# Kernel optimization log

Measured on AMD Instinct MI355X. Metric: run time of the kernel, lower is better.

The kernel has to match this reference:

```python
import jax, jax.numpy as jnp
import numpy as np

EPS = 1e-5

def _conv3x3(x, w):
    # x: [n,c,h,w], w: [o,c,3,3], stride 1, padding 1 (SAME)
    return jax.lax.conv_general_dilated(x, w, (1, 1), 'SAME',
                                        dimension_numbers=('NCHW', 'OIHW', 'NCHW'))

def _bn(x, g, b, m, v):
    # inference-mode BatchNorm2d with running stats
    s = g / jnp.sqrt(v + EPS)
    return x * s[:, None, None] + (b - m * s)[:, None, None]

def _lrelu(x):
    return jnp.where(x > 0, x, 0.2 * x)

def _conv1x1(x, w, b):
    # w: [o,c] (1x1 conv kernel collapsed)
    return jnp.einsum('nchw,oc->nohw', x, w) + b[:, None, None]

def _conv_relu(x, w, g, b, m, v):
    return _lrelu(_bn(_conv3x3(x, w), g, b, m, v))

def _pam(f, Wq, bq, Wk, bk, Wv, bv, alpha):
    n, c, h, w = f.shape
    hw = h * w
    q = _conv1x1(f, Wq, bq).reshape(n, -1, hw)   # [n,cr,hw]
    k = _conv1x1(f, Wk, bk).reshape(n, -1, hw)   # [n,cr,hw]
    # attention[i,j] over spatial tokens, softmax along j
    attn = jax.nn.softmax(jnp.einsum('nci,ncj->nij', q, k), axis=-1)  # [n,hw,hw]
    v = _conv1x1(f, Wv, bv).reshape(n, c, hw)    # [n,c,hw]
    # torch: bmm(v, attn^T) -> out[:, :, i] = sum_j v[:, :, j] * attn[i, j]
    out = jnp.einsum('ncj,nij->nci', v, attn).reshape(n, c, h, w)
    return alpha * out + f

def _cam(f, W1, b1, W2, b2):
    s = jnp.mean(f, axis=(2, 3), keepdims=True)  # AdaptiveAvgPool2d(1)
    s = _lrelu(_conv1x1(s, W1, b1))
    s = jax.nn.sigmoid(_conv1x1(s, W2, b2))
    return f * s

def _upx2(x):
    n, c, h, w = x.shape
    return jax.image.resize(x, (n, c, 2 * h, 2 * w), 'bilinear')

def setup_inputs() -> dict:
    key = jax.random.key(0)
    ks = jax.random.split(key, 16)
    N, C, H, W_ = 4, 512, 64, 64
    CR, NC = C // 8, 64
    f32 = jnp.float32
    def nrm(k, shape, s=0.05):
        return jax.random.normal(k, shape, f32) * s
    return {
        'x': jax.random.normal(ks[0], (N, C, H, W_), f32),
        'W_pam_in': nrm(ks[1], (C, C, 3, 3)),
        'pam_gamma': jnp.ones((C,), f32), 'pam_beta': jnp.zeros((C,), f32),
        'pam_mean': nrm(ks[2], (C,)), 'pam_var': jax.random.uniform(ks[3], (C,), f32) + 0.5,
        'Wq': nrm(ks[4], (CR, C)), 'bq': jnp.zeros((CR,), f32),
        'Wk': nrm(ks[5], (CR, C)), 'bk': jnp.zeros((CR,), f32),
        'Wv': nrm(ks[6], (C, C)), 'bv': jnp.zeros((C,), f32),
        'alpha': nrm(ks[7], (1,), 1.0),
        'W_pam_out': nrm(ks[8], (NC, C)), 'b_pam_out': jnp.zeros((NC,), f32),
        'W_cam_in': nrm(ks[9], (C, C, 3, 3)),
        'cam_gamma': jnp.ones((C,), f32), 'cam_beta': jnp.zeros((C,), f32),
        'cam_mean': nrm(ks[10], (C,)), 'cam_var': jax.random.uniform(ks[11], (C,), f32) + 0.5,
        'Wc1': nrm(ks[12], (CR, C)), 'bc1': jnp.zeros((CR,), f32),
        'Wc2': nrm(ks[13], (C, CR)), 'bc2': jnp.zeros((C,), f32),
        'W_cam_out': nrm(ks[14], (NC, C)), 'b_cam_out': jnp.zeros((NC,), f32),
    }

def reference(x, W_pam_in, pam_gamma, pam_beta, pam_mean, pam_var,
              Wq, bq, Wk, bk, Wv, bv, alpha, W_pam_out, b_pam_out,
              W_cam_in, cam_gamma, cam_beta, cam_mean, cam_var,
              Wc1, bc1, Wc2, bc2, W_cam_out, b_cam_out):
    pam_feat = _conv_relu(x, W_pam_in, pam_gamma, pam_beta, pam_mean, pam_var)
    pam_feat = _pam(pam_feat, Wq, bq, Wk, bk, Wv, bv, alpha)
    pam_feat = _upx2(_conv1x1(pam_feat, W_pam_out, b_pam_out))
    cam_feat = _conv_relu(x, W_cam_in, cam_gamma, cam_beta, cam_mean, cam_var)
    cam_feat = _cam(cam_feat, Wc1, bc1, Wc2, bc2)
    cam_feat = _upx2(_conv1x1(cam_feat, W_cam_out, b_cam_out))
    return pam_feat + cam_feat
```

## Files before the change

### kernel.cpp

```cpp
#include <hip/hip_runtime.h>
#include <hip/hip_bf16.h>
#include <math.h>

#define N_  4
#define C_  512
#define H_  64
#define W_  64
#define HW_ 4096
#define CR_ 64
#define NC_ 64
#define EPSV 1e-5f

typedef __attribute__((ext_vector_type(8))) __bf16 bf16x8;
typedef __attribute__((ext_vector_type(4))) float f32x4;
typedef __hip_bfloat16 bf16s;

__device__ __forceinline__ unsigned short bfb(float f) {
    union { bf16s h; unsigned short u; } cv;
    cv.h = __float2bfloat16(f);
    return cv.u;
}

__device__ __forceinline__ int swz8(int row, int ch) {
    return row * 64 + ((ch ^ (row & 7)) << 3);
}

__global__ __launch_bounds__(256) void k_xpose(
    const float* __restrict__ x, bf16s* __restrict__ xbT)
{
    __shared__ float xs[64][65];
    const int tid = threadIdx.x;
    const int n = blockIdx.z, c0 = blockIdx.y * 64, p0 = blockIdx.x * 64;
    for (int e = tid; e < 4096; e += 256) {
        int ci = e >> 6, pi = e & 63;
        xs[ci][pi] = x[((size_t)(n*C_ + c0 + ci))*HW_ + p0 + pi];
    }
    __syncthreads();
    for (int e = tid; e < 4096; e += 256) {
        int pi = e >> 6, ci = e & 63;
        xbT[((size_t)n*HW_ + p0 + pi)*C_ + c0 + ci] = __float2bfloat16(xs[ci][pi]);
    }
}

__global__ __launch_bounds__(256) void k_wprep(
    const float* __restrict__ w, bf16s* __restrict__ wb)
{
    int e = blockIdx.x * 256 + threadIdx.x;
    int c = e & 511; int r = e >> 9;
    int tap = r % 9; int o = r / 9;
    wb[e] = __float2bfloat16(w[((size_t)o*C_ + c)*9 + tap]);
}

__global__ __launch_bounds__(256) void k_wcast(
    const float* __restrict__ in, bf16s* __restrict__ out, int nElem)
{
    int e = blockIdx.x * 256 + threadIdx.x;
    if (e < nElem) out[e] = __float2bfloat16(in[e]);
}

__global__ __launch_bounds__(256, 2) void k_conv3x3_mfma(
    const bf16s* __restrict__ xbT, const bf16s* __restrict__ wb,
    const float* __restrict__ gamma, const float* __restrict__ beta,
    const float* __restrict__ mean, const float* __restrict__ var,
    float* __restrict__ out, bf16s* __restrict__ featT,
    float* __restrict__ csum, int mode)
{
    __shared__ bf16s aL[3][128][36];
    __shared__ bf16s bL[132][36];
    const int tid = threadIdx.x;
    const int n  = blockIdx.z;
    const int o0 = blockIdx.y * 128;
    const int pt = blockIdx.x;
    const int y0 = pt * 2;
    const int lane = tid & 63;
    const int wid  = tid >> 6;
    const int wr = wid >> 1, wc = wid & 1;
    const int lr = lane & 15, cb = lane >> 4;

    const int ao  = tid >> 2;
    const int ac  = (tid & 3) * 8;
    const int t0  = tid >> 2;
    const int t1  = t0 + 64;
    const int t2  = t0 + 128;
    const int ry1 = t1 >= 66 ? 1 : 0;
    const int xi1 = t1 - (ry1 ? 66 : 0);

    f32x4 acc[4][4];
#pragma unroll
    for (int i = 0; i < 4; ++i)
#pragma unroll
        for (int j = 0; j < 4; ++j) acc[i][j] = (f32x4){0.f,0.f,0.f,0.f};

    int4 pA0, pA1, pA2, pA3, pA4, pA5, pB0, pB1, pB2;

#define CONV_AADDR(DXI, OHALF, C0, DYI) \
    (const int4*)(wb + ((size_t)(o0 + (OHALF) + ao)*9 + (DYI)*3 + (DXI))*C_ + (C0) + ac)

#define CONV_BLOAD(DST, RY, XI, C0, DYI, VALID)                               \
    {                                                                         \
        int row_ = y0 + (DYI) - 1 + (RY);                                     \
        int xc_  = (XI) - 1;                                                  \
        int4 v_ = {0,0,0,0};                                                  \
        if ((VALID) && row_ >= 0 && row_ < H_ && xc_ >= 0 && xc_ < W_)        \
            v_ = *(const int4*)(xbT +                                         \
                ((size_t)n*HW_ + row_*W_ + xc_)*C_ + (C0) + ac);              \
        DST = v_;                                                             \
    }

#define CONV_ISSUE(C0, DYI)                                                   \
    {                                                                         \
        pA0 = *CONV_AADDR(0,  0, C0, DYI);                                    \
        pA1 = *CONV_AADDR(0, 64, C0, DYI);                                    \
        pA2 = *CONV_AADDR(1,  0, C0, DYI);                                    \
        pA3 = *CONV_AADDR(1, 64, C0, DYI);                                    \
        pA4 = *CONV_AADDR(2,  0, C0, DYI);                                    \
        pA5 = *CONV_AADDR(2, 64, C0, DYI);                                    \
        CONV_BLOAD(pB0, 0, t0, C0, DYI, 1)                                    \
        CONV_BLOAD(pB1, ry1, xi1, C0, DYI, 1)                                 \
        CONV_BLOAD(pB2, 1, t2 - 66, C0, DYI, tid < 16)                        \
    }

    CONV_ISSUE(0, 0)
    int c0 = 0, dyi = 0;
    for (int it = 0; it < 48; ++it) {
        *(int4*)&aL[0][ao][ac]      = pA0;
        *(int4*)&aL[0][64 + ao][ac] = pA1;
        *(int4*)&aL[1][ao][ac]      = pA2;
        *(int4*)&aL[1][64 + ao][ac] = pA3;
        *(int4*)&aL[2][ao][ac]      = pA4;
        *(int4*)&aL[2][64 + ao][ac] = pA5;
        *(int4*)&bL[t0][ac] = pB0;
        *(int4*)&bL[t1][ac] = pB1;
        if (tid < 16) *(int4*)&bL[t2][ac] = pB2;
        __syncthreads();
        int nd = dyi + 1, nc = c0;
        if (nd == 3) { nd = 0; nc += 32; }
        if (it < 47) CONV_ISSUE(nc, nd)
#pragma unroll
        for (int dxi = 0; dxi < 3; ++dxi) {
            bf16x8 af[4], bfv[4];
#pragma unroll
            for (int fm = 0; fm < 4; ++fm)
                af[fm] = *(const bf16x8*)&aL[dxi][wr*64 + fm*16 + lr][cb*8];
#pragma unroll
            for (int fn = 0; fn < 4; ++fn) {
                int pg = wc*64 + fn*16 + lr;
                int ry = pg >> 6, xc = pg & 63;
                bfv[fn] = *(const bf16x8*)&bL[ry*66 + xc + dxi][cb*8];
            }
#pragma unroll
            for (int fm = 0; fm < 4; ++fm)
#pragma unroll
                for (int fn = 0; fn < 4; ++fn)
                    acc[fm][fn] = __builtin_amdgcn_mfma_f32_16x16x32_bf16(
                        af[fm], bfv[fn], acc[fm][fn], 0, 0, 0);
        }
        __syncthreads();
        c0 = nc; dyi = nd;
    }
#undef CONV_ISSUE
#undef CONV_BLOAD
#undef CONV_AADDR
#pragma unroll
    for (int fm = 0; fm < 4; ++fm) {
        float sc[4], sh[4];
        const int obase = o0 + wr*64 + fm*16 + cb*4;
#pragma unroll
        for (int r = 0; r < 4; ++r) {
            int o = obase + r;
            sc[r] = gamma[o] * rsqrtf(var[o] + EPSV);
            sh[r] = beta[o] - mean[o]*sc[r];
        }
        float ps[4] = {0.f, 0.f, 0.f, 0.f};
#pragma unroll
        for (int fn = 0; fn < 4; ++fn) {
            int pg = wc*64 + fn*16 + lr;
            int p  = pt*128 + pg;
            float vv[4];
#pragma unroll
            for (int r = 0; r < 4; ++r) {
                float t = fmaf(acc[fm][fn][r], sc[r], sh[r]);
                vv[r] = t > 0.f ? t : 0.2f*t;
                if (mode == 0)
                    out[((size_t)(n*C_ + obase + r))*HW_ + p] = vv[r];
                else
                    ps[r] += vv[r];
            }
            uint2 u;
            u.x = (unsigned)bfb(vv[0]) | ((unsigned)bfb(vv[1]) << 16);
            u.y = (unsigned)bfb(vv[2]) | ((unsigned)bfb(vv[3]) << 16);
            *(uint2*)&featT[((size_t)n*HW_ + p)*C_ + obase] = u;
        }
        if (mode != 0) {
#pragma unroll
            for (int r = 0; r < 4; ++r) {
                float s = ps[r];
                s += __shfl_xor(s, 1);
                s += __shfl_xor(s, 2);
                s += __shfl_xor(s, 4);
                s += __shfl_xor(s, 8);
                if (lr == 0) atomicAdd(&csum[n*C_ + obase + r], s);
            }
        }
    }
}

__global__ __launch_bounds__(256, 2) void k_gemm(
    const bf16s* __restrict__ A, const bf16s* __restrict__ Bt,
    const float* __restrict__ bias, const float* __restrict__ scale,
    void* __restrict__ outp, int O, int mode)
{
    __shared__ bf16s aL[64][36];
    __shared__ bf16s bL[256][36];
    const int tid = threadIdx.x;
    const int n  = blockIdx.z;
    const int p0 = blockIdx.x * 256;
    const int o0 = blockIdx.y * 64;
    const int lane = tid & 63;
    const int wid  = tid >> 6;
    const int lr = lane & 15, cb = lane >> 4;
    const int arow = tid >> 2, ach = (tid & 3) * 8;

    f32x4 acc[4][4];
#pragma unroll
    for (int i = 0; i < 4; ++i)
#pragma unroll
        for (int j = 0; j < 4; ++j) acc[i][j] = (f32x4){0.f,0.f,0.f,0.f};

    int4 pA, pB0, pB1, pB2, pB3;
    float4 pS0, pS1;

#define GEMM_ISSUE(C0)                                                        \
    {                                                                         \
        pA = *(const int4*)&A[(size_t)(o0 + arow)*C_ + (C0) + ach];           \
        if (scale) {                                                          \
            pS0 = *(const float4*)&scale[(size_t)n*C_ + (C0) + ach];          \
            pS1 = *(const float4*)&scale[(size_t)n*C_ + (C0) + ach + 4];      \
        }                                                                     \
        pB0 = *(const int4*)&Bt[((size_t)n*HW_ + p0 + arow      )*C_ + (C0) + ach]; \
        pB1 = *(const int4*)&Bt[((size_t)n*HW_ + p0 + arow +  64)*C_ + (C0) + ach]; \
        pB2 = *(const int4*)&Bt[((size_t)n*HW_ + p0 + arow + 128)*C_ + (C0) + ach]; \
        pB3 = *(const int4*)&Bt[((size_t)n*HW_ + p0 + arow + 192)*C_ + (C0) + ach]; \
    }

    GEMM_ISSUE(0)
    for (int c0 = 0; c0 < C_; c0 += 32) {
        if (scale) {
            const bf16s* sp = (const bf16s*)&pA;
            bf16s tmp[8];
            tmp[0] = __float2bfloat16(__bfloat162float(sp[0]) * pS0.x);
            tmp[1] = __float2bfloat16(__bfloat162float(sp[1]) * pS0.y);
            tmp[2] = __float2bfloat16(__bfloat162float(sp[2]) * pS0.z);
            tmp[3] = __float2bfloat16(__bfloat162float(sp[3]) * pS0.w);
            tmp[4] = __float2bfloat16(__bfloat162float(sp[4]) * pS1.x);
            tmp[5] = __float2bfloat16(__bfloat162float(sp[5]) * pS1.y);
            tmp[6] = __float2bfloat16(__bfloat162float(sp[6]) * pS1.z);
            tmp[7] = __float2bfloat16(__bfloat162float(sp[7]) * pS1.w);
            *(int4*)&aL[arow][ach] = *(int4*)tmp;
        } else {
            *(int4*)&aL[arow][ach] = pA;
        }
        *(int4*)&bL[arow      ][ach] = pB0;
        *(int4*)&bL[arow +  64][ach] = pB1;
        *(int4*)&bL[arow + 128][ach] = pB2;
        *(int4*)&bL[arow + 192][ach] = pB3;
        __syncthreads();
        if (c0 + 32 < C_) GEMM_ISSUE(c0 + 32)
        bf16x8 af[4], bfv[4];
#pragma unroll
        for (int fo = 0; fo < 4; ++fo)
            af[fo] = *(const bf16x8*)&aL[fo*16 + lr][cb*8];
#pragma unroll
        for (int fp = 0; fp < 4; ++fp)
            bfv[fp] = *(const bf16x8*)&bL[wid*64 + fp*16 + lr][cb*8];
#pragma unroll
        for (int fo = 0; fo < 4; ++fo)
#pragma unroll
            for (int fp = 0; fp < 4; ++fp)
                acc[fo][fp] = __builtin_amdgcn_mfma_f32_16x16x32_bf16(
                    af[fo], bfv[fp], acc[fo][fp], 0, 0, 0);
        __syncthreads();
    }
#undef GEMM_ISSUE
#pragma unroll
    for (int fo = 0; fo < 4; ++fo) {
        const int obase = o0 + fo*16 + cb*4;
        float bv[4];
#pragma unroll
        for (int r = 0; r < 4; ++r) bv[r] = bias[obase + r];
#pragma unroll
        for (int fp = 0; fp < 4; ++fp) {
            int p = p0 + wid*64 + fp*16 + lr;
            float v[4];
#pragma unroll
            for (int r = 0; r < 4; ++r) v[r] = acc[fo][fp][r] + bv[r];
            if (mode == 1) {
                uint2 u;
                u.x = (unsigned)bfb(v[0]) | ((unsigned)bfb(v[1]) << 16);
                u.y = (unsigned)bfb(v[2]) | ((unsigned)bfb(v[3]) << 16);
                *(uint2*)&((bf16s*)outp)[((size_t)n*HW_ + p)*O + (obase - o0)] = u;
            } else if (mode == 2) {
#pragma unroll
                for (int r = 0; r < 4; ++r)
                    ((bf16s*)outp)[((size_t)(n*O + obase + r))*HW_ + p] =
                        __float2bfloat16(v[r]);
            } else {
#pragma unroll
                for (int r = 0; r < 4; ++r)
                    ((float*)outp)[((size_t)(n*O + obase + r))*HW_ + p] = v[r];
            }
        }
    }
}

__global__ __launch_bounds__(256) void k_rowstats_mfma(
    const bf16s* __restrict__ qb, const bf16s* __restrict__ kb,
    float* __restrict__ rowm, float* __restrict__ rowl)
{
    __shared__ bf16s qs[4096];
    __shared__ bf16s ks[2][4096];
    const int tid = threadIdx.x;
    const int lid = blockIdx.x + (blockIdx.y << 6) + (blockIdx.z << 8);
    const int n  = lid & 3;
    const int jz = (lid >> 2) & 1;
    const int i0 = (lid >> 3) << 6;
    const int lane = tid & 63;
    const int wid  = tid >> 6;
    const int lr = lane & 15, cb = lane >> 4;

    for (int e = tid; e < 512; e += 256) {
        int row = e >> 3, ch = e & 7;
        *(int4*)&qs[swz8(row, ch)] =
            *(const int4*)&qb[((size_t)n*HW_ + i0 + row)*CR_ + ch*8];
    }
    const int krow = tid >> 3, kch = tid & 7;
    const bf16s* kbase = kb + (size_t)n*HW_*CR_ + (size_t)jz*2048*CR_ + kch*8;
    int4 kreg0 = *(const int4*)(kbase + (size_t)krow*CR_);
    int4 kreg1 = *(const int4*)(kbase + (size_t)(krow + 32)*CR_);
    *(int4*)&ks[0][swz8(krow, kch)] = kreg0;
    *(int4*)&ks[0][swz8(krow + 32, kch)] = kreg1;
    kreg0 = *(const int4*)(kbase + (size_t)(64 + krow)*CR_);
    kreg1 = *(const int4*)(kbase + (size_t)(64 + krow + 32)*CR_);
    __syncthreads();
    bf16x8 bq[2];
#pragma unroll
    for (int kk = 0; kk < 2; ++kk)
        bq[kk] = *(const bf16x8*)&qs[swz8(wid*16 + lr, kk*4 + cb)];

    float m_t = -INFINITY, l_t = 0.f;
    for (int t = 0; t < 32; ++t) {
        const bf16s* kst = ks[t & 1];
        f32x4 sv[4];
#pragma unroll
        for (int fj = 0; fj < 4; ++fj) {
            f32x4 s = (f32x4){0.f,0.f,0.f,0.f};
#pragma unroll
            for (int kk = 0; kk < 2; ++kk) {
                bf16x8 ak = *(const bf16x8*)&kst[swz8(fj*16 + lr, kk*4 + cb)];
                s = __builtin_amdgcn_mfma_f32_16x16x32_bf16(ak, bq[kk], s, 0, 0, 0);
            }
            sv[fj] = s;
        }
        if (t < 31) {
            *(int4*)&ks[(t + 1) & 1][swz8(krow, kch)] = kreg0;
            *(int4*)&ks[(t + 1) & 1][swz8(krow + 32, kch)] = kreg1;
            if (t < 30) {
                kreg0 = *(const int4*)(kbase + (size_t)((t+2)*64 + krow)*CR_);
                kreg1 = *(const int4*)(kbase + (size_t)((t+2)*64 + krow + 32)*CR_);
            }
        }
        float mx = m_t;
#pragma unroll
        for (int fj = 0; fj < 4; ++fj)
#pragma unroll
            for (int r = 0; r < 4; ++r) mx = fmaxf(mx, sv[fj][r]);
        float sum = 0.f;
#pragma unroll
        for (int fj = 0; fj < 4; ++fj)
#pragma unroll
            for (int r = 0; r < 4; ++r) sum += __expf(sv[fj][r] - mx);
        l_t = l_t * __expf(m_t - mx) + sum;
        m_t = mx;
        __syncthreads();
    }
#pragma unroll
    for (int mask = 16; mask <= 32; mask <<= 1) {
        float mo = __shfl_xor(m_t, mask);
        float lo = __shfl_xor(l_t, mask);
        float m2 = fmaxf(m_t, mo);
        l_t = l_t * __expf(m_t - m2) + lo * __expf(mo - m2);
        m_t = m2;
    }
    if (cb == 0) {
        rowm[((size_t)jz*N_ + n)*HW_ + i0 + wid*16 + lr] = m_t;
        rowl[((size_t)jz*N_ + n)*HW_ + i0 + wid*16 + lr] = l_t;
    }
}

__global__ __launch_bounds__(256, 4) void k_pv_mfma(
    const bf16s* __restrict__ qb, const bf16s* __restrict__ kb,
    const bf16s* __restrict__ vb, const float* __restrict__ rowm,
    const float* __restrict__ rowl, const float* __restrict__ alpha,
    const float* __restrict__ feat, bf16s* __restrict__ featT)
{
    __shared__ bf16s ks[2][4096];
    __shared__ bf16s ps[2][4096];
    const int tid = threadIdx.x;
    const int lid = blockIdx.x + (blockIdx.y << 6) + (blockIdx.z << 8);
    const int k8  = lid & 7;
    const int n   = k8 >> 1;
    const int cc0 = (((lid >> 3) & 1) * 2 + (k8 & 1)) << 7;
    const int i0  = (lid >> 4) << 6;
    const int lane = tid & 63;
    const int wid  = tid >> 6;
    const int lr = lane & 15, cb = lane >> 4;

    for (int e = tid; e < 512; e += 256) {
        int row = e >> 3, ch = e & 7;
        *(int4*)&ks[0][swz8(row, ch)] =
            *(const int4*)&qb[((size_t)n*HW_ + i0 + row)*CR_ + ch*8];
    }
    const int krow = tid >> 3, kch = tid & 7;
    const bf16s* kbase = kb + (size_t)n*HW_*CR_ + kch*8;
    int4 kreg0 = *(const int4*)(kbase + (size_t)krow*CR_);
    int4 kreg1 = *(const int4*)(kbase + (size_t)(krow + 32)*CR_);
    __syncthreads();
    bf16x8 bq[2];
#pragma unroll
    for (int kk = 0; kk < 2; ++kk)
        bq[kk] = *(const bf16x8*)&ks[0][swz8(wid*16 + lr, kk*4 + cb)];

    const size_t sidx = (size_t)n*HW_ + i0 + wid*16 + lr;
    const float m0 = rowm[sidx], m1 = rowm[sidx + (size_t)N_*HW_];
    const float l0 = rowl[sidx], l1 = rowl[sidx + (size_t)N_*HW_];
    const float mreg = fmaxf(m0, m1);
    const float rinv = 1.f / (l0*__expf(m0 - mreg) + l1*__expf(m1 - mreg));
    const float al = alpha[0];
    __syncthreads();
    *(int4*)&ks[0][swz8(krow, kch)] = kreg0;
    *(int4*)&ks[0][swz8(krow + 32, kch)] = kreg1;
    kreg0 = *(const int4*)(kbase + (size_t)(64 + krow)*CR_);
    kreg1 = *(const int4*)(kbase + (size_t)(64 + krow + 32)*CR_);
    __syncthreads();

    f32x4 acc[2][4];
#pragma unroll
    for (int i = 0; i < 2; ++i)
#pragma unroll
        for (int j = 0; j < 4; ++j) acc[i][j] = (f32x4){0.f,0.f,0.f,0.f};

    const bf16s* vbase = vb + ((size_t)(n*C_ + cc0 + wid*32))*HW_;
    bf16x8 vc0, vc1, vc2, vc3, vn0, vn1, vn2, vn3;

    for (int jt = 0; jt < 64; ++jt) {
        const bf16s* vj = vbase + jt*64;
        vn0 = *(const bf16x8*)(vj + (size_t)(     lr)*HW_      + cb*8);
        vn1 = *(const bf16x8*)(vj + (size_t)(16 + lr)*HW_      + cb*8);
        vn2 = *(const bf16x8*)(vj + (size_t)(     lr)*HW_ + 32 + cb*8);
        vn3 = *(const bf16x8*)(vj + (size_t)(16 + lr)*HW_ + 32 + cb*8);
        if (jt > 0) {
            const bf16s* pp = ps[(jt - 1) & 1];
            bf16x8 pa[4];
#pragma unroll
            for (int fi = 0; fi < 4; ++fi)
                pa[fi] = *(const bf16x8*)&pp[swz8(fi*16 + lr, cb)];
#pragma unroll
            for (int fi = 0; fi < 4; ++fi) {
                acc[0][fi] = __builtin_amdgcn_mfma_f32_16x16x32_bf16(
                    vc0, pa[fi], acc[0][fi], 0, 0, 0);
                acc[1][fi] = __builtin_amdgcn_mfma_f32_16x16x32_bf16(
                    vc1, pa[fi], acc[1][fi], 0, 0, 0);
            }
#pragma unroll
            for (int fi = 0; fi < 4; ++fi)
                pa[fi] = *(const bf16x8*)&pp[swz8(fi*16 + lr, 4 + cb)];
#pragma unroll
            for (int fi = 0; fi < 4; ++fi) {
                acc[0][fi] = __builtin_amdgcn_mfma_f32_16x16x32_bf16(
                    vc2, pa[fi], acc[0][fi], 0, 0, 0);
                acc[1][fi] = __builtin_amdgcn_mfma_f32_16x16x32_bf16(
                    vc3, pa[fi], acc[1][fi], 0, 0, 0);
            }
        }
        {
            const bf16s* kst = ks[jt & 1];
            bf16s* pst = ps[jt & 1];
#pragma unroll
            for (int fj = 0; fj < 4; ++fj) {
                f32x4 s = (f32x4){0.f,0.f,0.f,0.f};
#pragma unroll
                for (int kk = 0; kk < 2; ++kk) {
                    bf16x8 ak = *(const bf16x8*)&kst[swz8(fj*16 + lr, kk*4 + cb)];
                    s = __builtin_amdgcn_mfma_f32_16x16x32_bf16(ak, bq[kk], s, 0, 0, 0);
                }
                unsigned short b[4];
#pragma unroll
                for (int r = 0; r < 4; ++r)
                    b[r] = bfb(__expf(s[r] - mreg) * rinv);
                uint2 u;
                u.x = (unsigned)b[0] | ((unsigned)b[1] << 16);
                u.y = (unsigned)b[2] | ((unsigned)b[3] << 16);
                *(uint2*)&pst[swz8(wid*16 + lr, fj*2 + (cb >> 1)) + (cb & 1)*4] = u;
            }
        }
        if (jt < 63) {
            *(int4*)&ks[(jt + 1) & 1][swz8(krow, kch)] = kreg0;
            *(int4*)&ks[(jt + 1) & 1][swz8(krow + 32, kch)] = kreg1;
            if (jt < 62) {
                kreg0 = *(const int4*)(kbase + (size_t)((jt+2)*64 + krow)*CR_);
                kreg1 = *(const int4*)(kbase + (size_t)((jt+2)*64 + krow + 32)*CR_);
            }
        }
        vc0 = vn0; vc1 = vn1; vc2 = vn2; vc3 = vn3;
        __syncthreads();
    }
    {
        const bf16s* pp = ps[63 & 1];
        bf16x8 pa[4];
#pragma unroll
        for (int fi = 0; fi < 4; ++fi)
            pa[fi] = *(const bf16x8*)&pp[swz8(fi*16 + lr, cb)];
#pragma unroll
        for (int fi = 0; fi < 4; ++fi) {
            acc[0][fi] = __builtin_amdgcn_mfma_f32_16x16x32_bf16(
                vc0, pa[fi], acc[0][fi], 0, 0, 0);
            acc[1][fi] = __builtin_amdgcn_mfma_f32_16x16x32_bf16(
                vc1, pa[fi], acc[1][fi], 0, 0, 0);
        }
#pragma unroll
        for (int fi = 0; fi < 4; ++fi)
            pa[fi] = *(const bf16x8*)&pp[swz8(fi*16 + lr, 4 + cb)];
#pragma unroll
        for (int fi = 0; fi < 4; ++fi) {
            acc[0][fi] = __builtin_amdgcn_mfma_f32_16x16x32_bf16(
                vc2, pa[fi], acc[0][fi], 0, 0, 0);
            acc[1][fi] = __builtin_amdgcn_mfma_f32_16x16x32_bf16(
                vc3, pa[fi], acc[1][fi], 0, 0, 0);
        }
    }
#pragma unroll
    for (int fc2 = 0; fc2 < 2; ++fc2) {
        const int ccl = wid*32 + fc2*16 + cb*4;
#pragma unroll
        for (int fi = 0; fi < 4; ++fi) {
            const int p = i0 + fi*16 + lr;
            const float* fp = &feat[((size_t)(n*C_ + cc0 + ccl))*HW_ + p];
            float v0 = fmaf(al, acc[fc2][fi][0], fp[0]);
            float v1 = fmaf(al, acc[fc2][fi][1], fp[(size_t)HW_]);
            float v2 = fmaf(al, acc[fc2][fi][2], fp[(size_t)2*HW_]);
            float v3 = fmaf(al, acc[fc2][fi][3], fp[(size_t)3*HW_]);
            uint2 u;
            u.x = (unsigned)bfb(v0) | ((unsigned)bfb(v1) << 16);
            u.y = (unsigned)bfb(v2) | ((unsigned)bfb(v3) << 16);
            *(uint2*)&featT[((size_t)n*HW_ + p)*C_ + cc0 + ccl] = u;
        }
    }
}

__global__ __launch_bounds__(64) void k_cmlp(
    const float* __restrict__ s0, const float* __restrict__ Wc1,
    const float* __restrict__ bc1, const float* __restrict__ Wc2,
    const float* __restrict__ bc2, float* __restrict__ s2)
{
    const int n = blockIdx.x, tid = threadIdx.x;
    __shared__ float s1s[64];
    float a = 0.f;
    for (int c = 0; c < C_; ++c)
        a = fmaf(Wc1[(size_t)tid*C_ + c], s0[n*C_ + c] * (1.f/HW_), a);
    a += bc1[tid];
    a = a > 0.f ? a : 0.2f*a;
    s1s[tid] = a;
    __syncthreads();
    for (int c = tid; c < C_; c += 64) {
        float b = 0.f;
        for (int i = 0; i < CR_; ++i) b = fmaf(Wc2[(size_t)c*CR_ + i], s1s[i], b);
        b += bc2[c];
        s2[n*C_ + c] = 1.f / (1.f + __expf(-b));
    }
}

__global__ __launch_bounds__(256) void k_up(
    const float* __restrict__ pl, const float* __restrict__ cl,
    float* __restrict__ out)
{
    int idx = blockIdx.x * 256 + threadIdx.x;
    int ox = idx & 127; int rest = idx >> 7;
    int oy = rest & 127; rest >>= 7;
    int o  = rest & 63;  int n = rest >> 6;
    float fy = oy*0.5f - 0.25f;
    float fx = ox*0.5f - 0.25f;
    int y0 = (int)floorf(fy); float wy = fy - y0;
    int x0 = (int)floorf(fx); float wx = fx - x0;
    int y0c = y0 < 0 ? 0 : y0;      int y1c = y0+1 > 63 ? 63 : y0+1;
    int x0c = x0 < 0 ? 0 : x0;      int x1c = x0+1 > 63 ? 63 : x0+1;
    const float* a = pl + ((size_t)(n*NC_ + o))*HW_;
    const float* b = cl + ((size_t)(n*NC_ + o))*HW_;
    float v00 = a[y0c*64+x0c] + b[y0c*64+x0c];
    float v01 = a[y0c*64+x1c] + b[y0c*64+x1c];
    float v10 = a[y1c*64+x0c] + b[y1c*64+x0c];
    float v11 = a[y1c*64+x1c] + b[y1c*64+x1c];
    out[idx] = (1.f-wy)*((1.f-wx)*v00 + wx*v01) + wy*((1.f-wx)*v10 + wx*v11);
}

extern "C" void kernel_launch(void* const* d_in, const int* in_sizes, int n_in,
                              void* d_out, int out_size, void* d_ws, size_t ws_size,
                              hipStream_t stream)
{
    const float* x         = (const float*)d_in[0];
    const float* W_pam_in  = (const float*)d_in[1];
    const float* pam_g     = (const float*)d_in[2];
    const float* pam_b     = (const float*)d_in[3];
    const float* pam_m     = (const float*)d_in[4];
    const float* pam_v     = (const float*)d_in[5];
    const float* Wq        = (const float*)d_in[6];
    const float* bq        = (const float*)d_in[7];
    const float* Wk        = (const float*)d_in[8];
    const float* bk        = (const float*)d_in[9];
    const float* Wv        = (const float*)d_in[10];
    const float* bv        = (const float*)d_in[11];
    const float* alpha     = (const float*)d_in[12];
    const float* W_pam_out = (const float*)d_in[13];
    const float* b_pam_out = (const float*)d_in[14];
    const float* W_cam_in  = (const float*)d_in[15];
    const float* cam_g     = (const float*)d_in[16];
    const float* cam_b     = (const float*)d_in[17];
    const float* cam_m     = (const float*)d_in[18];
    const float* cam_v     = (const float*)d_in[19];
    const float* Wc1       = (const float*)d_in[20];
    const float* bc1       = (const float*)d_in[21];
    const float* Wc2       = (const float*)d_in[22];
    const float* bc2       = (const float*)d_in[23];
    const float* W_cam_out = (const float*)d_in[24];
    const float* b_cam_out = (const float*)d_in[25];

    float* feat    = (float*)d_ws;
    float* pam_low = feat    + 8388608;
    float* rowm    = pam_low + 1048576;
    float* rowl    = rowm    + 32768;
    float* s0      = rowl    + 32768;
    float* s2      = s0      + 2048;
    bf16s* xbT     = (bf16s*)(s2 + 2048);
    bf16s* featTb  = xbT + 8388608;
    bf16s* vb      = featTb + 8388608;
    bf16s* qb      = vb + 8388608;
    bf16s* kb      = qb + 1048576;
    bf16s* wbp     = kb + 1048576;
    bf16s* Wqb     = wbp + 2359296;
    bf16s* Wkb     = Wqb + 32768;
    bf16s* Wvb     = Wkb + 32768;
    bf16s* Wpob    = Wvb + 262144;
    bf16s* Wcob    = Wpob + 32768;
    float* cam_low = (float*)qb;

    dim3 b256(256);
    k_xpose<<<dim3(64,8,4), b256, 0, stream>>>(x, xbT);
    k_wcast<<<dim3(128), b256, 0, stream>>>(Wq, Wqb, 32768);
    k_wcast<<<dim3(128), b256, 0, stream>>>(Wk, Wkb, 32768);
    k_wcast<<<dim3(1024), b256, 0, stream>>>(Wv, Wvb, 262144);
    k_wcast<<<dim3(128), b256, 0, stream>>>(W_pam_out, Wpob, 32768);
    k_wcast<<<dim3(128), b256, 0, stream>>>(W_cam_out, Wcob, 32768);
    hipMemsetAsync(s0, 0, 2048*sizeof(float), stream);
    k_wprep<<<dim3(9216), b256, 0, stream>>>(W_pam_in, wbp);
    k_conv3x3_mfma<<<dim3(32,4,4), b256, 0, stream>>>(
        xbT, wbp, pam_g, pam_b, pam_m, pam_v, feat, featTb, nullptr, 0);
    k_gemm<<<dim3(16,1,4), b256, 0, stream>>>(Wqb, featTb, bq, nullptr, qb, 64, 1);
    k_gemm<<<dim3(16,1,4), b256, 0, stream>>>(Wkb, featTb, bk, nullptr, kb, 64, 1);
    k_gemm<<<dim3(16,8,4), b256, 0, stream>>>(Wvb, featTb, bv, nullptr, vb, 512, 2);
    k_rowstats_mfma<<<dim3(64,4,2), b256, 0, stream>>>(qb, kb, rowm, rowl);
    k_pv_mfma<<<dim3(64,4,4), b256, 0, stream>>>(
        qb, kb, vb, rowm, rowl, alpha, feat, featTb);
    k_gemm<<<dim3(16,1,4), b256, 0, stream>>>(
        Wpob, featTb, b_pam_out, nullptr, pam_low, 64, 0);
    k_wprep<<<dim3(9216), b256, 0, stream>>>(W_cam_in, wbp);
    k_conv3x3_mfma<<<dim3(32,4,4), b256, 0, stream>>>(
        xbT, wbp, cam_g, cam_b, cam_m, cam_v, feat, featTb, s0, 1);
    k_cmlp<<<dim3(4), dim3(64), 0, stream>>>(s0, Wc1, bc1, Wc2, bc2, s2);
    k_gemm<<<dim3(16,1,4), b256, 0, stream>>>(
        Wcob, featTb, b_cam_out, s2, cam_low, 64, 0);
    k_up<<<dim3(16384), b256, 0, stream>>>(pam_low, cam_low, (float*)d_out);
}
```

Before: 487.6 us.

## Fuse PAM and CAM 3x3 convs into one launch and merge Q/K projections

Both 3x3 conv branches now run in a single launch over a doubled grid, with each block selecting its weights, BN parameters and output buffer by half. The fp32 feature write is removed, and the PAM residual is read back from the bf16 transposed feature buffer instead. The Q and K 1x1 projections are merged into one GEMM that writes two contiguous outputs, and occupancy on the conv kernel is raised to 3 blocks per CU. These changes remove a large fp32 write and read, a kernel launch pair, and give the conv a fuller grid. In exchange the residual now carries bf16 precision and more workspace is used for the second feature and weight buffers.

```diff
diff --git a/kernel.cpp b/kernel.cpp
--- a/kernel.cpp
+++ b/kernel.cpp
@@ -21,6 +21,10 @@
     return cv.u;
 }
 
+__device__ __forceinline__ float b2f(unsigned short h) {
+    union { unsigned u; float f; } c; c.u = ((unsigned)h) << 16; return c.f;
+}
+
 __device__ __forceinline__ int swz8(int row, int ch) {
     return row * 64 + ((ch ^ (row & 7)) << 3);
 }
@@ -58,20 +62,30 @@
     if (e < nElem) out[e] = __float2bfloat16(in[e]);
 }
 
-__global__ __launch_bounds__(256, 2) void k_conv3x3_mfma(
-    const bf16s* __restrict__ xbT, const bf16s* __restrict__ wb,
-    const float* __restrict__ gamma, const float* __restrict__ beta,
-    const float* __restrict__ mean, const float* __restrict__ var,
-    float* __restrict__ out, bf16s* __restrict__ featT,
-    float* __restrict__ csum, int mode)
+__global__ __launch_bounds__(256, 3) void k_conv3x3_mfma(
+    const bf16s* __restrict__ xbT,
+    const bf16s* __restrict__ wb,  const bf16s* __restrict__ wb2,
+    const float* __restrict__ gamma,  const float* __restrict__ beta,
+    const float* __restrict__ mean,   const float* __restrict__ var,
+    const float* __restrict__ gamma2, const float* __restrict__ beta2,
+    const float* __restrict__ mean2,  const float* __restrict__ var2,
+    bf16s* __restrict__ featT, bf16s* __restrict__ featT2,
+    float* __restrict__ csum)
 {
     __shared__ bf16s aL[3][128][36];
     __shared__ bf16s bL[132][36];
     const int tid = threadIdx.x;
     const int n  = blockIdx.z;
-    const int o0 = blockIdx.y * 128;
+    const int half = blockIdx.y >> 2;
+    const int o0 = (blockIdx.y & 3) * 128;
     const int pt = blockIdx.x;
     const int y0 = pt * 2;
+    const bf16s* wbs = half ? wb2 : wb;
+    const float* gm = half ? gamma2 : gamma;
+    const float* bt = half ? beta2  : beta;
+    const float* mn = half ? mean2  : mean;
+    const float* vr = half ? var2   : var;
+    bf16s* ft = half ? featT2 : featT;
     const int lane = tid & 63;
     const int wid  = tid >> 6;
     const int wr = wid >> 1, wc = wid & 1;
@@ -94,7 +108,7 @@
     int4 pA0, pA1, pA2, pA3, pA4, pA5, pB0, pB1, pB2;
 
 #define CONV_AADDR(DXI, OHALF, C0, DYI) \
-    (const int4*)(wb + ((size_t)(o0 + (OHALF) + ao)*9 + (DYI)*3 + (DXI))*C_ + (C0) + ac)
+    (const int4*)(wbs + ((size_t)(o0 + (OHALF) + ao)*9 + (DYI)*3 + (DXI))*C_ + (C0) + ac)
 
 #define CONV_BLOAD(DST, RY, XI, C0, DYI, VALID)                               \
     {                                                                         \
@@ -168,8 +182,8 @@
 #pragma unroll
         for (int r = 0; r < 4; ++r) {
             int o = obase + r;
-            sc[r] = gamma[o] * rsqrtf(var[o] + EPSV);
-            sh[r] = beta[o] - mean[o]*sc[r];
+            sc[r] = gm[o] * rsqrtf(vr[o] + EPSV);
+            sh[r] = bt[o] - mn[o]*sc[r];
         }
         float ps[4] = {0.f, 0.f, 0.f, 0.f};
 #pragma unroll
@@ -181,17 +195,14 @@
             for (int r = 0; r < 4; ++r) {
                 float t = fmaf(acc[fm][fn][r], sc[r], sh[r]);
                 vv[r] = t > 0.f ? t : 0.2f*t;
-                if (mode == 0)
-                    out[((size_t)(n*C_ + obase + r))*HW_ + p] = vv[r];
-                else
-                    ps[r] += vv[r];
+                ps[r] += vv[r];
             }
             uint2 u;
             u.x = (unsigned)bfb(vv[0]) | ((unsigned)bfb(vv[1]) << 16);
             u.y = (unsigned)bfb(vv[2]) | ((unsigned)bfb(vv[3]) << 16);
-            *(uint2*)&featT[((size_t)n*HW_ + p)*C_ + obase] = u;
-        }
-        if (mode != 0) {
+            *(uint2*)&ft[((size_t)n*HW_ + p)*C_ + obase] = u;
+        }
+        if (half) {
 #pragma unroll
             for (int r = 0; r < 4; ++r) {
                 float s = ps[r];
@@ -207,7 +218,8 @@
 
 __global__ __launch_bounds__(256, 2) void k_gemm(
     const bf16s* __restrict__ A, const bf16s* __restrict__ Bt,
-    const float* __restrict__ bias, const float* __restrict__ scale,
+    const float* __restrict__ bias, const float* __restrict__ bias2,
+    const float* __restrict__ scale,
     void* __restrict__ outp, int O, int mode)
 {
     __shared__ bf16s aL[64][36];
@@ -285,20 +297,24 @@
 #pragma unroll
     for (int fo = 0; fo < 4; ++fo) {
         const int obase = o0 + fo*16 + cb*4;
+        const float* bp = (mode == 3 && (obase >> 6)) ? bias2 : bias;
+        const int bofs = (mode == 3) ? (obase & 63) : obase;
         float bv[4];
 #pragma unroll
-        for (int r = 0; r < 4; ++r) bv[r] = bias[obase + r];
+        for (int r = 0; r < 4; ++r) bv[r] = bp[bofs + r];
 #pragma unroll
         for (int fp = 0; fp < 4; ++fp) {
             int p = p0 + wid*64 + fp*16 + lr;
             float v[4];
 #pragma unroll
             for (int r = 0; r < 4; ++r) v[r] = acc[fo][fp][r] + bv[r];
-            if (mode == 1) {
+            if (mode == 3) {
                 uint2 u;
                 u.x = (unsigned)bfb(v[0]) | ((unsigned)bfb(v[1]) << 16);
                 u.y = (unsigned)bfb(v[2]) | ((unsigned)bfb(v[3]) << 16);
-                *(uint2*)&((bf16s*)outp)[((size_t)n*HW_ + p)*O + (obase - o0)] = u;
+                size_t base = (((size_t)((obase >> 6) * N_ + n))*HW_ + p)*64
+                              + (obase & 63);
+                *(uint2*)&((bf16s*)outp)[base] = u;
             } else if (mode == 2) {
 #pragma unroll
                 for (int r = 0; r < 4; ++r)
@@ -401,7 +417,7 @@
     const bf16s* __restrict__ qb, const bf16s* __restrict__ kb,
     const bf16s* __restrict__ vb, const float* __restrict__ rowm,
     const float* __restrict__ rowl, const float* __restrict__ alpha,
-    const float* __restrict__ feat, bf16s* __restrict__ featT)
+    bf16s* __restrict__ featT)
 {
     __shared__ bf16s ks[2][4096];
     __shared__ bf16s ps[2][4096];
@@ -544,15 +560,20 @@
 #pragma unroll
         for (int fi = 0; fi < 4; ++fi) {
             const int p = i0 + fi*16 + lr;
-            const float* fp = &feat[((size_t)(n*C_ + cc0 + ccl))*HW_ + p];
-            float v0 = fmaf(al, acc[fc2][fi][0], fp[0]);
-            float v1 = fmaf(al, acc[fc2][fi][1], fp[(size_t)HW_]);
-            float v2 = fmaf(al, acc[fc2][fi][2], fp[(size_t)2*HW_]);
-            float v3 = fmaf(al, acc[fc2][fi][3], fp[(size_t)3*HW_]);
+            bf16s* fb = &featT[((size_t)n*HW_ + p)*C_ + cc0 + ccl];
+            uint2 fv = *(const uint2*)fb;
+            float f0 = b2f((unsigned short)(fv.x & 0xffff));
+            float f1 = b2f((unsigned short)(fv.x >> 16));
+            float f2 = b2f((unsigned short)(fv.y & 0xffff));
+            float f3 = b2f((unsigned short)(fv.y >> 16));
+            float v0 = fmaf(al, acc[fc2][fi][0], f0);
+            float v1 = fmaf(al, acc[fc2][fi][1], f1);
+            float v2 = fmaf(al, acc[fc2][fi][2], f2);
+            float v3 = fmaf(al, acc[fc2][fi][3], f3);
             uint2 u;
             u.x = (unsigned)bfb(v0) | ((unsigned)bfb(v1) << 16);
             u.y = (unsigned)bfb(v2) | ((unsigned)bfb(v3) << 16);
-            *(uint2*)&featT[((size_t)n*HW_ + p)*C_ + cc0 + ccl] = u;
+            *(uint2*)fb = u;
         }
     }
 }
@@ -633,19 +654,20 @@
     const float* W_cam_out = (const float*)d_in[24];
     const float* b_cam_out = (const float*)d_in[25];
 
-    float* feat    = (float*)d_ws;
-    float* pam_low = feat    + 8388608;
+    float* pam_low = (float*)d_ws;
     float* rowm    = pam_low + 1048576;
     float* rowl    = rowm    + 32768;
     float* s0      = rowl    + 32768;
     float* s2      = s0      + 2048;
     bf16s* xbT     = (bf16s*)(s2 + 2048);
     bf16s* featTb  = xbT + 8388608;
-    bf16s* vb      = featTb + 8388608;
+    bf16s* featTb2 = featTb + 8388608;
+    bf16s* vb      = featTb2 + 8388608;
     bf16s* qb      = vb + 8388608;
     bf16s* kb      = qb + 1048576;
     bf16s* wbp     = kb + 1048576;
-    bf16s* Wqb     = wbp + 2359296;
+    bf16s* wbp2    = wbp + 2359296;
+    bf16s* Wqb     = wbp2 + 2359296;
     bf16s* Wkb     = Wqb + 32768;
     bf16s* Wvb     = Wkb + 32768;
     bf16s* Wpob    = Wvb + 262144;
@@ -661,21 +683,21 @@
     k_wcast<<<dim3(128), b256, 0, stream>>>(W_cam_out, Wcob, 32768);
     hipMemsetAsync(s0, 0, 2048*sizeof(float), stream);
     k_wprep<<<dim3(9216), b256, 0, stream>>>(W_pam_in, wbp);
-    k_conv3x3_mfma<<<dim3(32,4,4), b256, 0, stream>>>(
-        xbT, wbp, pam_g, pam_b, pam_m, pam_v, feat, featTb, nullptr, 0);
-    k_gemm<<<dim3(16,1,4), b256, 0, stream>>>(Wqb, featTb, bq, nullptr, qb, 64, 1);
-    k_gemm<<<dim3(16,1,4), b256, 0, stream>>>(Wkb, featTb, bk, nullptr, kb, 64, 1);
-    k_gemm<<<dim3(16,8,4), b256, 0, stream>>>(Wvb, featTb, bv, nullptr, vb, 512, 2);
+    k_wprep<<<dim3(9216), b256, 0, stream>>>(W_cam_in, wbp2);
+    k_conv3x3_mfma<<<dim3(32,8,4), b256, 0, stream>>>(
+        xbT, wbp, wbp2, pam_g, pam_b, pam_m, pam_v,
+        cam_g, cam_b, cam_m, cam_v, featTb, featTb2, s0);
+    k_gemm<<<dim3(16,2,4), b256, 0, stream>>>(
+        Wqb, featTb, bq, bk, nullptr, qb, 128, 3);
+    k_gemm<<<dim3(16,8,4), b256, 0, stream>>>(
+        Wvb, featTb, bv, nullptr, nullptr, vb, 512, 2);
     k_rowstats_mfma<<<dim3(64,4,2), b256, 0, stream>>>(qb, kb, rowm, rowl);
     k_pv_mfma<<<dim3(64,4,4), b256, 0, stream>>>(
-        qb, kb, vb, rowm, rowl, alpha, feat, featTb);
+        qb, kb, vb, rowm, rowl, alpha, featTb);
     k_gemm<<<dim3(16,1,4), b256, 0, stream>>>(
-        Wpob, featTb, b_pam_out, nullptr, pam_low, 64, 0);
-    k_wprep<<<dim3(9216), b256, 0, stream>>>(W_cam_in, wbp);
-    k_conv3x3_mfma<<<dim3(32,4,4), b256, 0, stream>>>(
-        xbT, wbp, cam_g, cam_b, cam_m, cam_v, feat, featTb, s0, 1);
+        Wpob, featTb, b_pam_out, nullptr, nullptr, pam_low, 64, 0);
     k_cmlp<<<dim3(4), dim3(64), 0, stream>>>(s0, Wc1, bc1, Wc2, bc2, s2);
     k_gemm<<<dim3(16,1,4), b256, 0, stream>>>(
-        Wcob, featTb, b_cam_out, s2, cam_low, 64, 0);
+        Wcob, featTb2, b_cam_out, nullptr, s2, cam_low, 64, 0);
     k_up<<<dim3(16384), b256, 0, stream>>>(pam_low, cam_low, (float*)d_out);
 }
```

Measured after the change: 465.7 us. -4.5%, faster.
